# Kernel optimization log

Hardware: AMD Instinct MI355X
Metric: run time of the kernel (lower is better)

## Reference

```python
import jax, jax.numpy as jnp
import numpy as np
from jax import lax

EPS = 1e-5
C = 232          # inp == oup
BF = C // 2      # branch_features
GROUPS = 2


def bn(x, g, b, m, v):
    # inference batchnorm over channel axis 1 of NCHW
    scale = g / jnp.sqrt(v + EPS)
    return x * scale[None, :, None, None] + (b - m * scale)[None, :, None, None]


def prelu(x, a):
    return jnp.where(x >= 0, x, a.reshape(()) * x)


def conv1x1(x, w):
    # x: [B,C,H,W], w: [O,C]
    return jnp.einsum('bchw,oc->bohw', x, w)


def dwconv3x3(x, w):
    # depthwise 3x3, stride 1, pad 1; w: [C,1,3,3]
    return lax.conv_general_dilated(
        x, w, window_strides=(1, 1), padding=((1, 1), (1, 1)),
        feature_group_count=x.shape[1],
        dimension_numbers=('NCHW', 'OIHW', 'NCHW'))


def setup_inputs() -> dict:
    key = jax.random.key(0)
    ks = jax.random.split(key, 12)
    B, H, W = 64, 56, 56
    inp = {
        'x': jax.random.normal(ks[0], (B, C, H, W), jnp.float32),
        'w2': jax.random.normal(ks[1], (BF, BF), jnp.float32) * 0.1,
        'bn1_g': jax.random.uniform(ks[2], (BF,), jnp.float32, 0.5, 1.5),
        'bn1_b': jax.random.normal(ks[3], (BF,), jnp.float32) * 0.1,
        'bn1_m': jax.random.normal(ks[4], (BF,), jnp.float32) * 0.1,
        'bn1_v': jax.random.uniform(ks[5], (BF,), jnp.float32, 0.5, 1.5),
        'alpha1': jnp.full((1,), 0.25, jnp.float32),
        'wdw': jax.random.normal(ks[6], (BF, 1, 3, 3), jnp.float32) * 0.1,
        'bn2_g': jax.random.uniform(ks[7], (BF,), jnp.float32, 0.5, 1.5),
        'bn2_b': jax.random.normal(ks[8], (BF,), jnp.float32) * 0.1,
        'bn2_m': jax.random.normal(ks[9], (BF,), jnp.float32) * 0.1,
        'bn2_v': jax.random.uniform(ks[10], (BF,), jnp.float32, 0.5, 1.5),
        'w3': jax.random.normal(ks[11], (BF, BF), jnp.float32) * 0.1,
        'bn3_g': jax.random.uniform(jax.random.fold_in(key, 101), (BF,), jnp.float32, 0.5, 1.5),
        'bn3_b': jax.random.normal(jax.random.fold_in(key, 102), (BF,)) * 0.1,
        'bn3_m': jax.random.normal(jax.random.fold_in(key, 103), (BF,)) * 0.1,
        'bn3_v': jax.random.uniform(jax.random.fold_in(key, 104), (BF,), jnp.float32, 0.5, 1.5),
        'alpha2': jnp.full((1,), 0.25, jnp.float32),
    }
    return inp


def reference(x, w2, bn1_g, bn1_b, bn1_m, bn1_v, alpha1, wdw,
              bn2_g, bn2_b, bn2_m, bn2_v, w3, bn3_g, bn3_b, bn3_m, bn3_v, alpha2):
    # stride == 1 path: split channels in half
    x1, x2 = x[:, :BF], x[:, BF:]
    # branch2: 1x1 conv -> BN -> PReLU -> dw3x3 -> BN -> 1x1 conv -> BN -> PReLU
    h = prelu(bn(conv1x1(x2, w2), bn1_g, bn1_b, bn1_m, bn1_v), alpha1)
    h = bn(dwconv3x3(h, wdw), bn2_g, bn2_b, bn2_m, bn2_v)
    h = prelu(bn(conv1x1(h, w3), bn3_g, bn3_b, bn3_m, bn3_v), alpha2)
    out = jnp.concatenate([x1, h], axis=1)
    # channel shuffle (groups=2): out channel k reads input channel (k%2)*cpg + k//2
    cpg = C // GROUPS
    idx = (jnp.arange(C) % GROUPS) * cpg + jnp.arange(C) // GROUPS
    return out[:, idx]
```

## Files before the change

kernel.cpp:

```cpp
#include <hip/hip_runtime.h>
#include <hip/hip_bf16.h>


#define BATCH 64
#define CTOT  232
#define BFC   116
#define HW    3136
#define WD    56
#define CP    128
#define EPSV  1e-5f

typedef unsigned short u16;
typedef __attribute__((ext_vector_type(8))) short short8;
typedef __attribute__((ext_vector_type(4))) float float4v;

__device__ __forceinline__ u16 f2bf(float f) {
    union { float f; unsigned u; } v; v.f = f;
    unsigned r = v.u + 0x7FFF + ((v.u >> 16) & 1);
    return (u16)(r >> 16);
}
__device__ __forceinline__ float bf2f(u16 u) {
    union { unsigned u; float f; } v; v.u = ((unsigned)u) << 16;
    return v.f;
}

__global__ __launch_bounds__(256) void shuffle_copy(const float* __restrict__ x,
                                                    float* __restrict__ out) {
    int bc = blockIdx.x;
    int b = bc / BFC, c = bc % BFC;
    const float4v* src = (const float4v*)(x + ((size_t)b * CTOT + c) * HW);
    float4v* dst = (float4v*)(out + ((size_t)b * CTOT + 2 * c) * HW);
    for (int i = threadIdx.x; i < HW / 4; i += 256) dst[i] = src[i];
}

__global__ __launch_bounds__(256) void conv1_kernel(
    const float* __restrict__ x, const float* __restrict__ w2,
    const float* __restrict__ g1, const float* __restrict__ b1,
    const float* __restrict__ m1, const float* __restrict__ v1,
    const float* __restrict__ al1, u16* __restrict__ h1) {
    __shared__ __align__(16) u16 aF[8 * 4 * 64 * 8];
    __shared__ __align__(16) u16 bF[8 * 4 * 64 * 8];
    int tid = threadIdx.x;
    int p0 = blockIdx.x * 128;
    int b = blockIdx.y;
    const float* x2 = x + ((size_t)b * CTOT + BFC) * HW;

    {
        int c_off = tid >> 7;
        int pp = tid & 127;
        int p = p0 + pp;
        bool pv = p < HW;
        int mt = pp >> 4, lsub = pp & 15;
        for (int cb = 0; cb < CP; cb += 2) {
            int c = cb + c_off;
            float val = (pv && c < BFC) ? x2[(size_t)c * HW + p] : 0.f;
            int kt = c >> 5;
            int lane = (((c >> 3) & 3) << 4) | lsub;
            aF[(((mt << 2) + kt) * 64 + lane) * 8 + (c & 7)] = f2bf(val);
        }
    }
    {
        int lane = tid & 63, w = tid >> 6;
        for (int fid = w; fid < 32; fid += 4) {
            int nt = fid >> 2, kt = fid & 3;
            int o = nt * 16 + (lane & 15);
            int cb = kt * 32 + ((lane >> 4) << 3);
            short8 vv;
            for (int j = 0; j < 8; j++) {
                int c = cb + j;
                float val = (o < BFC && c < BFC) ? w2[o * BFC + c] : 0.f;
                ((u16*)&vv)[j] = f2bf(val);
            }
            *(short8*)&bF[(fid * 64 + lane) * 8] = vv;
        }
    }
    __syncthreads();

    int lane = tid & 63, w = tid >> 6;
    short8 a0[4], a1[4];
    for (int kt = 0; kt < 4; kt++) {
        a0[kt] = *(const short8*)&aF[(((2 * w) * 4 + kt) * 64 + lane) * 8];
        a1[kt] = *(const short8*)&aF[(((2 * w + 1) * 4 + kt) * 64 + lane) * 8];
    }
    float a1s = al1[0];
    u16* h1p = h1 + (size_t)b * HW * CP;
    for (int nt = 0; nt < 8; nt++) {
        float4v acc0 = {0.f, 0.f, 0.f, 0.f}, acc1 = {0.f, 0.f, 0.f, 0.f};
        for (int kt = 0; kt < 4; kt++) {
            short8 bb = *(const short8*)&bF[((nt * 4 + kt) * 64 + lane) * 8];
            acc0 = __builtin_amdgcn_mfma_f32_16x16x32_bf16(a0[kt], bb, acc0, 0, 0, 0);
            acc1 = __builtin_amdgcn_mfma_f32_16x16x32_bf16(a1[kt], bb, acc1, 0, 0, 0);
        }
        int o = nt * 16 + (lane & 15);
        float sc = 0.f, sh = 0.f;
        if (o < BFC) {
            sc = g1[o] * rsqrtf(v1[o] + EPSV);
            sh = b1[o] - m1[o] * sc;
        }
        for (int half = 0; half < 2; half++) {
            float4v acc = half ? acc1 : acc0;
            int mt = 2 * w + half;
            int prow = p0 + mt * 16 + ((lane >> 4) << 2);
            for (int r = 0; r < 4; r++) {
                int p = prow + r;
                if (p < HW) {
                    float y = 0.f;
                    if (o < BFC) {
                        y = acc[r] * sc + sh;
                        y = y >= 0.f ? y : a1s * y;
                    }
                    h1p[(size_t)p * CP + o] = f2bf(y);
                }
            }
        }
    }
}

__global__ __launch_bounds__(256) void conv2_kernel(
    const u16* __restrict__ h1, const float* __restrict__ wdw,
    const float* __restrict__ g2, const float* __restrict__ b2,
    const float* __restrict__ m2, const float* __restrict__ v2,
    const float* __restrict__ w3,
    const float* __restrict__ g3, const float* __restrict__ b3,
    const float* __restrict__ m3, const float* __restrict__ v3,
    const float* __restrict__ al2, float* __restrict__ out) {
    __shared__ __align__(16) u16 h2F[7 * 4 * 64 * 8];
    __shared__ __align__(16) u16 reg1[8 * 4 * 64 * 8];
    int tid = threadIdx.x;
    int b = blockIdx.y;
    int r0 = blockIdx.x * 2;
    int p0 = r0 * WD;
    float* f1 = (float*)reg1;

    for (int idx = tid; idx < 1152 + 256; idx += 256) {
        if (idx < 1152) {
            int tap = idx >> 7, c = idx & 127;
            f1[idx] = (c < BFC) ? wdw[c * 9 + tap] : 0.f;
        } else if (idx < 1280) {
            int c = idx - 1152;
            f1[1152 + c] = (c < BFC) ? g2[c] * rsqrtf(v2[c] + EPSV) : 0.f;
        } else {
            int c = idx - 1280;
            float sh = 0.f;
            if (c < BFC) { float sc = g2[c] * rsqrtf(v2[c] + EPSV); sh = b2[c] - m2[c] * sc; }
            f1[1280 + c] = sh;
        }
    }
    __syncthreads();

    const u16* h1b = h1 + (size_t)b * HW * CP;
    for (int it = 0; it < 7; it++) {
        int t = it * 256 + tid;
        int g = t & 15, pl = t >> 4;
        int rr = (pl >= WD) ? 1 : 0;
        int col = pl - rr * WD;
        int row = r0 + rr;
        float acc[8];
        for (int j = 0; j < 8; j++) acc[j] = 0.f;
        for (int dy = -1; dy <= 1; dy++) {
            int y = row + dy;
            if (y < 0 || y >= WD) continue;
            for (int dx = -1; dx <= 1; dx++) {
                int xc = col + dx;
                if (xc < 0 || xc >= WD) continue;
                int tap = (dy + 1) * 3 + (dx + 1);
                short8 hv = *(const short8*)(h1b + ((size_t)(y * WD + xc)) * CP + g * 8);
                const u16* us = (const u16*)&hv;
                const float* wv = &f1[tap * 128 + g * 8];
                for (int j = 0; j < 8; j++) acc[j] += bf2f(us[j]) * wv[j];
            }
        }
        short8 hv;
        for (int j = 0; j < 8; j++) {
            int c = g * 8 + j;
            ((u16*)&hv)[j] = f2bf(acc[j] * f1[1152 + c] + f1[1280 + c]);
        }
        int mt = pl >> 4, kt = g >> 2;
        int lane = ((g & 3) << 4) | (pl & 15);
        *(short8*)&h2F[((mt * 4 + kt) * 64 + lane) * 8] = hv;
    }
    __syncthreads();

    int lane = tid & 63, w = tid >> 6;
    for (int fid = w; fid < 32; fid += 4) {
        int nt = fid >> 2, kt = fid & 3;
        int o = nt * 16 + (lane & 15);
        int cb = kt * 32 + ((lane >> 4) << 3);
        short8 vv;
        for (int j = 0; j < 8; j++) {
            int c = cb + j;
            float val = (o < BFC && c < BFC) ? w3[o * BFC + c] : 0.f;
            ((u16*)&vv)[j] = f2bf(val);
        }
        *(short8*)&reg1[(fid * 64 + lane) * 8] = vv;
    }
    __syncthreads();

    float a2s = al2[0];
    short8 bf0[2][4];
    for (int i = 0; i < 2; i++)
        for (int kt = 0; kt < 4; kt++)
            bf0[i][kt] = *(const short8*)&reg1[(((2 * w + i) * 4 + kt) * 64 + lane) * 8];
    for (int mt = 0; mt < 7; mt++) {
        short8 af[4];
        for (int kt = 0; kt < 4; kt++)
            af[kt] = *(const short8*)&h2F[((mt * 4 + kt) * 64 + lane) * 8];
        for (int i = 0; i < 2; i++) {
            float4v acc = {0.f, 0.f, 0.f, 0.f};
            for (int kt = 0; kt < 4; kt++)
                acc = __builtin_amdgcn_mfma_f32_16x16x32_bf16(af[kt], bf0[i][kt], acc, 0, 0, 0);
            int nt = 2 * w + i;
            int o = nt * 16 + (lane & 15);
            if (o < BFC) {
                float sc = g3[o] * rsqrtf(v3[o] + EPSV);
                float sh = b3[o] - m3[o] * sc;
                int plb = mt * 16 + ((lane >> 4) << 2);
                float4v ov;
                for (int r = 0; r < 4; r++) {
                    float y = acc[r] * sc + sh;
                    ov[r] = y >= 0.f ? y : a2s * y;
                }
                *(float4v*)&out[((size_t)b * CTOT + 2 * o + 1) * HW + p0 + plb] = ov;
            }
        }
    }
}

extern "C" void kernel_launch(void* const* d_in, const int* in_sizes, int n_in,
                              void* d_out, int out_size, void* d_ws, size_t ws_size,
                              hipStream_t stream) {
    const float* x   = (const float*)d_in[0];
    const float* w2  = (const float*)d_in[1];
    const float* g1  = (const float*)d_in[2];
    const float* b1  = (const float*)d_in[3];
    const float* m1  = (const float*)d_in[4];
    const float* v1  = (const float*)d_in[5];
    const float* al1 = (const float*)d_in[6];
    const float* wdw = (const float*)d_in[7];
    const float* g2  = (const float*)d_in[8];
    const float* b2  = (const float*)d_in[9];
    const float* m2  = (const float*)d_in[10];
    const float* v2  = (const float*)d_in[11];
    const float* w3  = (const float*)d_in[12];
    const float* g3  = (const float*)d_in[13];
    const float* b3  = (const float*)d_in[14];
    const float* m3  = (const float*)d_in[15];
    const float* v3  = (const float*)d_in[16];
    const float* al2 = (const float*)d_in[17];
    float* out = (float*)d_out;
    u16* h1 = (u16*)d_ws;

    hipLaunchKernelGGL(shuffle_copy, dim3(BATCH * BFC), dim3(256), 0, stream, x, out);
    hipLaunchKernelGGL(conv1_kernel, dim3(25, BATCH), dim3(256), 0, stream,
                       x, w2, g1, b1, m1, v1, al1, h1);
    hipLaunchKernelGGL(conv2_kernel, dim3(28, BATCH), dim3(256), 0, stream,
                       h1, wdw, g2, b2, m2, v2, w3, g3, b3, m3, v3, al2, out);
}
```

Baseline: 596.3 us.

## Restructure pipeline: prefold BN into weights, fuse conv1+dwconv, merge shuffle copy into conv3

Adds a small prep kernel that folds the batchnorm scales into bf16 copies of w2/w3 and folds the BN2 shift into the conv3 bias. The first 1x1 conv is fused with the depthwise 3x3 conv, recomputing halo rows in shared memory so h1 never goes to global memory. The dwconv output is written with 120 channels instead of 128. The x1 shuffle copy becomes extra blocks in the final conv kernel, removing a launch. In exchange, halo rows are recomputed, x is loaded strided straight from global memory into registers, and the fused kernel uses heavy per-thread register arrays.

```diff
diff --git a/kernel.cpp b/kernel.cpp
--- a/kernel.cpp
+++ b/kernel.cpp
@@ -7,12 +7,19 @@
 #define BFC   116
 #define HW    3136
 #define WD    56
-#define CP    128
+#define CH2   120
 #define EPSV  1e-5f
 
 typedef unsigned short u16;
 typedef __attribute__((ext_vector_type(8))) short short8;
 typedef __attribute__((ext_vector_type(4))) float float4v;
+
+#define WS_W2P   0
+#define WS_W3P   32768
+#define WS_WDWT  65536
+#define WS_B1P   69888
+#define WS_B3P   70400
+#define WS_H2    131072
 
 __device__ __forceinline__ u16 f2bf(float f) {
     union { float f; unsigned u; } v; v.f = f;
@@ -24,203 +31,230 @@
     return v.f;
 }
 
-__global__ __launch_bounds__(256) void shuffle_copy(const float* __restrict__ x,
-                                                    float* __restrict__ out) {
-    int bc = blockIdx.x;
-    int b = bc / BFC, c = bc % BFC;
-    const float4v* src = (const float4v*)(x + ((size_t)b * CTOT + c) * HW);
-    float4v* dst = (float4v*)(out + ((size_t)b * CTOT + 2 * c) * HW);
-    for (int i = threadIdx.x; i < HW / 4; i += 256) dst[i] = src[i];
-}
-
-__global__ __launch_bounds__(256) void conv1_kernel(
-    const float* __restrict__ x, const float* __restrict__ w2,
-    const float* __restrict__ g1, const float* __restrict__ b1,
+__global__ __launch_bounds__(256) void prep(
+    const float* __restrict__ w2, const float* __restrict__ g1, const float* __restrict__ b1,
     const float* __restrict__ m1, const float* __restrict__ v1,
-    const float* __restrict__ al1, u16* __restrict__ h1) {
-    __shared__ __align__(16) u16 aF[8 * 4 * 64 * 8];
-    __shared__ __align__(16) u16 bF[8 * 4 * 64 * 8];
-    int tid = threadIdx.x;
-    int p0 = blockIdx.x * 128;
-    int b = blockIdx.y;
-    const float* x2 = x + ((size_t)b * CTOT + BFC) * HW;
-
-    {
-        int c_off = tid >> 7;
-        int pp = tid & 127;
-        int p = p0 + pp;
-        bool pv = p < HW;
-        int mt = pp >> 4, lsub = pp & 15;
-        for (int cb = 0; cb < CP; cb += 2) {
-            int c = cb + c_off;
-            float val = (pv && c < BFC) ? x2[(size_t)c * HW + p] : 0.f;
-            int kt = c >> 5;
-            int lane = (((c >> 3) & 3) << 4) | lsub;
-            aF[(((mt << 2) + kt) * 64 + lane) * 8 + (c & 7)] = f2bf(val);
-        }
-    }
-    {
-        int lane = tid & 63, w = tid >> 6;
-        for (int fid = w; fid < 32; fid += 4) {
-            int nt = fid >> 2, kt = fid & 3;
-            int o = nt * 16 + (lane & 15);
-            int cb = kt * 32 + ((lane >> 4) << 3);
-            short8 vv;
-            for (int j = 0; j < 8; j++) {
-                int c = cb + j;
-                float val = (o < BFC && c < BFC) ? w2[o * BFC + c] : 0.f;
-                ((u16*)&vv)[j] = f2bf(val);
-            }
-            *(short8*)&bF[(fid * 64 + lane) * 8] = vv;
-        }
-    }
-    __syncthreads();
-
-    int lane = tid & 63, w = tid >> 6;
-    short8 a0[4], a1[4];
-    for (int kt = 0; kt < 4; kt++) {
-        a0[kt] = *(const short8*)&aF[(((2 * w) * 4 + kt) * 64 + lane) * 8];
-        a1[kt] = *(const short8*)&aF[(((2 * w + 1) * 4 + kt) * 64 + lane) * 8];
-    }
-    float a1s = al1[0];
-    u16* h1p = h1 + (size_t)b * HW * CP;
-    for (int nt = 0; nt < 8; nt++) {
-        float4v acc0 = {0.f, 0.f, 0.f, 0.f}, acc1 = {0.f, 0.f, 0.f, 0.f};
-        for (int kt = 0; kt < 4; kt++) {
-            short8 bb = *(const short8*)&bF[((nt * 4 + kt) * 64 + lane) * 8];
-            acc0 = __builtin_amdgcn_mfma_f32_16x16x32_bf16(a0[kt], bb, acc0, 0, 0, 0);
-            acc1 = __builtin_amdgcn_mfma_f32_16x16x32_bf16(a1[kt], bb, acc1, 0, 0, 0);
-        }
-        int o = nt * 16 + (lane & 15);
-        float sc = 0.f, sh = 0.f;
-        if (o < BFC) {
-            sc = g1[o] * rsqrtf(v1[o] + EPSV);
-            sh = b1[o] - m1[o] * sc;
-        }
-        for (int half = 0; half < 2; half++) {
-            float4v acc = half ? acc1 : acc0;
-            int mt = 2 * w + half;
-            int prow = p0 + mt * 16 + ((lane >> 4) << 2);
-            for (int r = 0; r < 4; r++) {
-                int p = prow + r;
-                if (p < HW) {
-                    float y = 0.f;
-                    if (o < BFC) {
-                        y = acc[r] * sc + sh;
-                        y = y >= 0.f ? y : a1s * y;
-                    }
-                    h1p[(size_t)p * CP + o] = f2bf(y);
-                }
-            }
-        }
-    }
-}
-
-__global__ __launch_bounds__(256) void conv2_kernel(
-    const u16* __restrict__ h1, const float* __restrict__ wdw,
+    const float* __restrict__ wdw,
     const float* __restrict__ g2, const float* __restrict__ b2,
     const float* __restrict__ m2, const float* __restrict__ v2,
-    const float* __restrict__ w3,
-    const float* __restrict__ g3, const float* __restrict__ b3,
+    const float* __restrict__ w3, const float* __restrict__ g3, const float* __restrict__ b3,
     const float* __restrict__ m3, const float* __restrict__ v3,
-    const float* __restrict__ al2, float* __restrict__ out) {
-    __shared__ __align__(16) u16 h2F[7 * 4 * 64 * 8];
-    __shared__ __align__(16) u16 reg1[8 * 4 * 64 * 8];
+    char* __restrict__ ws) {
+    u16* w2p = (u16*)(ws + WS_W2P);
+    u16* w3p = (u16*)(ws + WS_W3P);
+    float* wdwt = (float*)(ws + WS_WDWT);
+    float* b1p = (float*)(ws + WS_B1P);
+    float* b3p = (float*)(ws + WS_B3P);
+    int tid = threadIdx.x;
+    int bx = blockIdx.x;
+    if (bx < 8) {
+        int o = bx * 16 + (tid >> 4);
+        int cs = (tid & 15) * 8;
+        float sc = (o < BFC) ? g1[o] * rsqrtf(v1[o] + EPSV) : 0.f;
+        short8 v;
+        for (int j = 0; j < 8; j++) {
+            int c = cs + j;
+            float val = (o < BFC && c < BFC) ? sc * w2[o * BFC + c] : 0.f;
+            ((u16*)&v)[j] = f2bf(val);
+        }
+        *(short8*)&w2p[o * 128 + cs] = v;
+    } else if (bx < 16) {
+        int o = (bx - 8) * 16 + (tid >> 4);
+        int cs = (tid & 15) * 8;
+        float sc = (o < BFC) ? g3[o] * rsqrtf(v3[o] + EPSV) : 0.f;
+        short8 v;
+        for (int j = 0; j < 8; j++) {
+            int c = cs + j;
+            float val = 0.f;
+            if (o < BFC && c < BFC) {
+                float sc2 = g2[c] * rsqrtf(v2[c] + EPSV);
+                val = sc * sc2 * w3[o * BFC + c];
+            }
+            ((u16*)&v)[j] = f2bf(val);
+        }
+        *(short8*)&w3p[o * 128 + cs] = v;
+    } else {
+        if (tid < CH2)
+            for (int tap = 0; tap < 9; tap++)
+                wdwt[tap * CH2 + tid] = (tid < BFC) ? wdw[tid * 9 + tap] : 0.f;
+        if (tid < 128) {
+            float b1v = 0.f, b3v = 0.f;
+            if (tid < BFC) {
+                float sc1 = g1[tid] * rsqrtf(v1[tid] + EPSV);
+                b1v = b1[tid] - m1[tid] * sc1;
+                float sc3 = g3[tid] * rsqrtf(v3[tid] + EPSV);
+                float s = 0.f;
+                for (int c = 0; c < BFC; c++) {
+                    float sc2 = g2[c] * rsqrtf(v2[c] + EPSV);
+                    float sh2 = b2[c] - m2[c] * sc2;
+                    s += w3[tid * BFC + c] * sh2;
+                }
+                b3v = (b3[tid] - m3[tid] * sc3) + sc3 * s;
+            }
+            b1p[tid] = b1v;
+            b3p[tid] = b3v;
+        }
+    }
+}
+
+__global__ __launch_bounds__(256, 3) void k1(const float* __restrict__ x,
+        const float* __restrict__ al1, char* __restrict__ ws) {
+    __shared__ u16 h1s[224 * CH2];
+    const u16* w2p = (const u16*)(ws + WS_W2P);
+    const float* wdwt = (const float*)(ws + WS_WDWT);
+    const float* b1p = (const float*)(ws + WS_B1P);
+    u16* h2g = (u16*)(ws + WS_H2);
+
+    int tid = threadIdx.x;
+    int lane = tid & 63;
+    int w = tid >> 6;
+    int l15 = lane & 15, kq = lane >> 4;
+    int b = blockIdx.y;
+    int r0 = blockIdx.x * 2;
+    int p_in0 = r0 * WD - WD;
+
+    const float* x2 = x + ((size_t)b * CTOT + BFC) * HW;
+    float a1 = al1[0];
+
+    int mh = w >> 1, nh = w & 1;
+    short8 bfr[4][4];
+    float biasv[4];
+    for (int ni = 0; ni < 4; ni++) {
+        int o = (nh * 4 + ni) * 16 + l15;
+        for (int kt = 0; kt < 4; kt++)
+            bfr[ni][kt] = *(const short8*)&w2p[o * 128 + kt * 32 + kq * 8];
+        biasv[ni] = b1p[o];
+    }
+    for (int mi = 0; mi < 7; mi++) {
+        int mt = mh * 7 + mi;
+        int p = p_in0 + mt * 16 + l15;
+        bool pv = (p >= 0) && (p < HW);
+        short8 afr[4];
+        for (int kt = 0; kt < 4; kt++) {
+            short8 av;
+            for (int j = 0; j < 8; j++) {
+                int c = kt * 32 + kq * 8 + j;
+                float v = 0.f;
+                if (pv && c < BFC) v = x2[(size_t)c * HW + p];
+                ((u16*)&av)[j] = f2bf(v);
+            }
+            afr[kt] = av;
+        }
+        for (int ni = 0; ni < 4; ni++) {
+            float4v acc = {0.f, 0.f, 0.f, 0.f};
+            for (int kt = 0; kt < 4; kt++)
+                acc = __builtin_amdgcn_mfma_f32_16x16x32_bf16(afr[kt], bfr[ni][kt], acc, 0, 0, 0);
+            int o = (nh * 4 + ni) * 16 + l15;
+            if (o < CH2) {
+                int plb = mt * 16 + kq * 4;
+                for (int r = 0; r < 4; r++) {
+                    int pl = plb + r;
+                    int pim = p_in0 + pl;
+                    float y = acc[r] + biasv[ni];
+                    y = y >= 0.f ? y : a1 * y;
+                    h1s[pl * CH2 + o] = (pim >= 0 && pim < HW) ? f2bf(y) : (u16)0;
+                }
+            }
+        }
+    }
+    __syncthreads();
+
+    for (int u = tid; u < 420; u += 256) {
+        int oct = u % 15;
+        int pq = u / 15;
+        int rr = pq / 14;
+        int col0 = (pq % 14) * 4;
+        float acc[4][8];
+        for (int i = 0; i < 4; i++)
+            for (int j = 0; j < 8; j++) acc[i][j] = 0.f;
+        for (int dy = 0; dy < 3; dy++) {
+            int lr = rr + dy;
+            float f[6][8];
+            for (int k = 0; k < 6; k++) {
+                int ci = col0 - 1 + k;
+                if (ci >= 0 && ci < WD) {
+                    short8 v = *(const short8*)&h1s[(lr * WD + ci) * CH2 + oct * 8];
+                    for (int j = 0; j < 8; j++) f[k][j] = bf2f(((const u16*)&v)[j]);
+                } else {
+                    for (int j = 0; j < 8; j++) f[k][j] = 0.f;
+                }
+            }
+            for (int dx = 0; dx < 3; dx++) {
+                const float* wt = &wdwt[(dy * 3 + dx) * CH2 + oct * 8];
+                float4v w0 = *(const float4v*)&wt[0];
+                float4v w1 = *(const float4v*)&wt[4];
+                float w8[8] = {w0[0], w0[1], w0[2], w0[3], w1[0], w1[1], w1[2], w1[3]};
+                for (int i = 0; i < 4; i++)
+                    for (int j = 0; j < 8; j++)
+                        acc[i][j] += f[i + dx][j] * w8[j];
+            }
+        }
+        int prow = (r0 + rr) * WD + col0;
+        u16* dst = h2g + ((size_t)b * HW + prow) * CH2 + oct * 8;
+        for (int i = 0; i < 4; i++) {
+            short8 ov;
+            for (int j = 0; j < 8; j++) ((u16*)&ov)[j] = f2bf(acc[i][j]);
+            *(short8*)&dst[(size_t)i * CH2] = ov;
+        }
+    }
+}
+
+__global__ __launch_bounds__(256) void k2(const float* __restrict__ x,
+        const float* __restrict__ al2, const char* __restrict__ ws,
+        float* __restrict__ out) {
     int tid = threadIdx.x;
     int b = blockIdx.y;
-    int r0 = blockIdx.x * 2;
-    int p0 = r0 * WD;
-    float* f1 = (float*)reg1;
-
-    for (int idx = tid; idx < 1152 + 256; idx += 256) {
-        if (idx < 1152) {
-            int tap = idx >> 7, c = idx & 127;
-            f1[idx] = (c < BFC) ? wdw[c * 9 + tap] : 0.f;
-        } else if (idx < 1280) {
-            int c = idx - 1152;
-            f1[1152 + c] = (c < BFC) ? g2[c] * rsqrtf(v2[c] + EPSV) : 0.f;
-        } else {
-            int c = idx - 1280;
-            float sh = 0.f;
-            if (c < BFC) { float sc = g2[c] * rsqrtf(v2[c] + EPSV); sh = b2[c] - m2[c] * sc; }
-            f1[1280 + c] = sh;
-        }
-    }
-    __syncthreads();
-
-    const u16* h1b = h1 + (size_t)b * HW * CP;
-    for (int it = 0; it < 7; it++) {
-        int t = it * 256 + tid;
-        int g = t & 15, pl = t >> 4;
-        int rr = (pl >= WD) ? 1 : 0;
-        int col = pl - rr * WD;
-        int row = r0 + rr;
-        float acc[8];
-        for (int j = 0; j < 8; j++) acc[j] = 0.f;
-        for (int dy = -1; dy <= 1; dy++) {
-            int y = row + dy;
-            if (y < 0 || y >= WD) continue;
-            for (int dx = -1; dx <= 1; dx++) {
-                int xc = col + dx;
-                if (xc < 0 || xc >= WD) continue;
-                int tap = (dy + 1) * 3 + (dx + 1);
-                short8 hv = *(const short8*)(h1b + ((size_t)(y * WD + xc)) * CP + g * 8);
-                const u16* us = (const u16*)&hv;
-                const float* wv = &f1[tap * 128 + g * 8];
-                for (int j = 0; j < 8; j++) acc[j] += bf2f(us[j]) * wv[j];
-            }
-        }
-        short8 hv;
-        for (int j = 0; j < 8; j++) {
-            int c = g * 8 + j;
-            ((u16*)&hv)[j] = f2bf(acc[j] * f1[1152 + c] + f1[1280 + c]);
-        }
-        int mt = pl >> 4, kt = g >> 2;
-        int lane = ((g & 3) << 4) | (pl & 15);
-        *(short8*)&h2F[((mt * 4 + kt) * 64 + lane) * 8] = hv;
-    }
-    __syncthreads();
-
+    int bx = blockIdx.x;
+    if (bx >= 25) {
+        int c0 = (bx - 25) * 15;
+        int c1 = c0 + 15 < BFC ? c0 + 15 : BFC;
+        for (int c = c0; c < c1; c++) {
+            const float4v* src = (const float4v*)(x + ((size_t)b * CTOT + c) * HW);
+            float4v* dst = (float4v*)(out + ((size_t)b * CTOT + 2 * c) * HW);
+            for (int i = tid; i < HW / 4; i += 256) dst[i] = src[i];
+        }
+        return;
+    }
+    const u16* w3p = (const u16*)(ws + WS_W3P);
+    const float* b3p = (const float*)(ws + WS_B3P);
+    const u16* h2g = (const u16*)(ws + WS_H2);
     int lane = tid & 63, w = tid >> 6;
-    for (int fid = w; fid < 32; fid += 4) {
-        int nt = fid >> 2, kt = fid & 3;
-        int o = nt * 16 + (lane & 15);
-        int cb = kt * 32 + ((lane >> 4) << 3);
-        short8 vv;
-        for (int j = 0; j < 8; j++) {
-            int c = cb + j;
-            float val = (o < BFC && c < BFC) ? w3[o * BFC + c] : 0.f;
-            ((u16*)&vv)[j] = f2bf(val);
-        }
-        *(short8*)&reg1[(fid * 64 + lane) * 8] = vv;
-    }
-    __syncthreads();
-
-    float a2s = al2[0];
-    short8 bf0[2][4];
-    for (int i = 0; i < 2; i++)
+    int l15 = lane & 15, kq = lane >> 4;
+    int p0 = bx * 128;
+    float a2 = al2[0];
+    short8 bfr[2][4];
+    float biasv[2];
+    for (int i = 0; i < 2; i++) {
+        int o = (2 * w + i) * 16 + l15;
         for (int kt = 0; kt < 4; kt++)
-            bf0[i][kt] = *(const short8*)&reg1[(((2 * w + i) * 4 + kt) * 64 + lane) * 8];
-    for (int mt = 0; mt < 7; mt++) {
-        short8 af[4];
-        for (int kt = 0; kt < 4; kt++)
-            af[kt] = *(const short8*)&h2F[((mt * 4 + kt) * 64 + lane) * 8];
+            bfr[i][kt] = *(const short8*)&w3p[o * 128 + kt * 32 + kq * 8];
+        biasv[i] = b3p[o];
+    }
+    const u16* h2b = h2g + (size_t)b * HW * CH2;
+    short8 z8 = {0, 0, 0, 0, 0, 0, 0, 0};
+    for (int mt = 0; mt < 8; mt++) {
+        int p = p0 + mt * 16 + l15;
+        bool pv = p < HW;
+        const u16* arow = h2b + (size_t)p * CH2;
+        short8 afr[4];
+        for (int kt = 0; kt < 4; kt++) {
+            short8 av = z8;
+            if (pv && !(kt == 3 && kq == 3)) av = *(const short8*)&arow[kt * 32 + kq * 8];
+            afr[kt] = av;
+        }
         for (int i = 0; i < 2; i++) {
             float4v acc = {0.f, 0.f, 0.f, 0.f};
             for (int kt = 0; kt < 4; kt++)
-                acc = __builtin_amdgcn_mfma_f32_16x16x32_bf16(af[kt], bf0[i][kt], acc, 0, 0, 0);
-            int nt = 2 * w + i;
-            int o = nt * 16 + (lane & 15);
-            if (o < BFC) {
-                float sc = g3[o] * rsqrtf(v3[o] + EPSV);
-                float sh = b3[o] - m3[o] * sc;
-                int plb = mt * 16 + ((lane >> 4) << 2);
+                acc = __builtin_amdgcn_mfma_f32_16x16x32_bf16(afr[kt], bfr[i][kt], acc, 0, 0, 0);
+            int o = (2 * w + i) * 16 + l15;
+            int pq = p0 + mt * 16 + kq * 4;
+            if (o < BFC && pq < HW) {
                 float4v ov;
                 for (int r = 0; r < 4; r++) {
-                    float y = acc[r] * sc + sh;
-                    ov[r] = y >= 0.f ? y : a2s * y;
-                }
-                *(float4v*)&out[((size_t)b * CTOT + 2 * o + 1) * HW + p0 + plb] = ov;
+                    float y = acc[r] + biasv[i];
+                    ov[r] = y >= 0.f ? y : a2 * y;
+                }
+                *(float4v*)&out[((size_t)b * CTOT + 2 * o + 1) * HW + pq] = ov;
             }
         }
     }
@@ -248,11 +282,10 @@
     const float* v3  = (const float*)d_in[16];
     const float* al2 = (const float*)d_in[17];
     float* out = (float*)d_out;
-    u16* h1 = (u16*)d_ws;
-
-    hipLaunchKernelGGL(shuffle_copy, dim3(BATCH * BFC), dim3(256), 0, stream, x, out);
-    hipLaunchKernelGGL(conv1_kernel, dim3(25, BATCH), dim3(256), 0, stream,
-                       x, w2, g1, b1, m1, v1, al1, h1);
-    hipLaunchKernelGGL(conv2_kernel, dim3(28, BATCH), dim3(256), 0, stream,
-                       h1, wdw, g2, b2, m2, v2, w3, g3, b3, m3, v3, al2, out);
-}
+    char* ws = (char*)d_ws;
+
+    hipLaunchKernelGGL(prep, dim3(17), dim3(256), 0, stream,
+                       w2, g1, b1, m1, v1, wdw, g2, b2, m2, v2, w3, g3, b3, m3, v3, ws);
+    hipLaunchKernelGGL(k1, dim3(28, BATCH), dim3(256), 0, stream, x, al1, ws);
+    hipLaunchKernelGGL(k2, dim3(33, BATCH), dim3(256), 0, stream, x, al2, ws, out);
+}
```

Measured after the change: 530.7 us. 1.12x faster.
